# Kernel tuning notes

Measured on AMD Instinct MI355X. Metric: run time of the kernel, lower is better.

Reference implementation:

```python
import jax, jax.numpy as jnp
import numpy as np

N, E = 50000, 800000
F_IN, F_OUT, H, F_EDGE = 256, 32, 8, 5
LEAKY_SLOPE = 0.2


def setup_inputs() -> dict:
    key = jax.random.key(0)
    ks = jax.random.split(key, 6)
    x = jax.random.normal(ks[0], (N, F_IN), dtype=jnp.float32)
    edge_index = jax.random.randint(ks[1], (2, E), 0, N, dtype=jnp.int64)
    edge_attr = jax.random.normal(ks[2], (E, F_EDGE), dtype=jnp.float32)
    degree_src = jax.random.randint(ks[3], (E,), 0, 64, dtype=jnp.int64)
    # Xavier-uniform params
    lim_W = float(np.sqrt(6.0 / (F_IN + F_OUT)))
    W = jax.random.uniform(ks[4], (H, F_IN, F_OUT), minval=-lim_W, maxval=lim_W, dtype=jnp.float32)
    A = 2 * F_OUT + F_EDGE
    lim_a = float(np.sqrt(6.0 / (H + A)))
    a = jax.random.uniform(ks[5], (H, A), minval=-lim_a, maxval=lim_a, dtype=jnp.float32)
    lim_e = float(np.sqrt(1.0 / F_EDGE))
    W_edge_w = jax.random.uniform(jax.random.fold_in(key, 7), (F_EDGE, F_EDGE), minval=-lim_e, maxval=lim_e, dtype=jnp.float32)
    return {"x": x, "edge_index": edge_index, "edge_attr": edge_attr,
            "degree_src": degree_src, "W": W, "a": a, "W_edge_w": W_edge_w}


def reference(x, edge_index, edge_attr, degree_src, W, a, W_edge_w):
    n = x.shape[0]
    h, f_out = W.shape[0], W.shape[2]
    src, dst = edge_index[0], edge_index[1]
    # per-head projection: (N, H, F_out)
    Wh = jnp.einsum('nf,hfo->nho', x, W)
    # split attention vector instead of materializing the concat
    a_src, a_dst, a_e = a[:, :f_out], a[:, f_out:2 * f_out], a[:, 2 * f_out:]
    ef = edge_attr @ W_edge_w.T                      # (E, F_edge)
    e = (jnp.einsum('eho,ho->eh', Wh[src], a_src)
         + jnp.einsum('eho,ho->eh', Wh[dst], a_dst)
         + ef @ a_e.T)                                # (E, H)
    e = jax.nn.leaky_relu(e, LEAKY_SLOPE)
    scale = 1.0 / jnp.sqrt(jnp.clip(degree_src.astype(jnp.float32), 1.0, None))
    e = e * scale[:, None]
    # segment softmax over src; torch scatter_reduce amax include_self=True with zeros init -> max includes 0
    e_max = jnp.maximum(jax.ops.segment_max(e, src, num_segments=n), 0.0)
    e_exp = jnp.exp(e - e_max[src])
    e_sum = jax.ops.segment_sum(e_exp, src, num_segments=n)
    alpha = e_exp / (e_sum[src] + 1e-16)             # (E, H)
    msg = Wh[dst] * alpha[:, :, None]                # (E, H, F_out)
    out = jax.ops.segment_sum(msg, src, num_segments=n)
    out = jax.nn.elu(out.reshape(n, h * f_out))
    return out, alpha
```

## Files before the change

kernel.cpp:

```cpp
#include <hip/hip_runtime.h>
#include <hip/hip_bf16.h>
#include <math.h>

#define NN 50000
#define NE 800000
#define FIN 256
#define FOUT 32
#define NH 8
#define FE 5
#define AROW 69

typedef float f32x4 __attribute__((ext_vector_type(4)));
typedef short bf16x8 __attribute__((ext_vector_type(8)));

static __device__ __forceinline__ unsigned short f2bf(float f) {
    unsigned u = __float_as_uint(f);
    unsigned r = (u + 0x7FFFu + ((u >> 16) & 1u)) >> 16;
    return (unsigned short)r;
}
static __device__ __forceinline__ float bf2f(unsigned short b) {
    return __uint_as_float(((unsigned)b) << 16);
}

__global__ void k_cmat(const float* __restrict__ a, const float* __restrict__ Wew,
                       float* __restrict__ C) {
    int t = threadIdx.x;
    if (t < NH * FE) {
        int h = t / FE, k = t % FE;
        float s = 0.f;
        for (int j = 0; j < FE; ++j) s += a[h * AROW + 2 * FOUT + j] * Wew[j * FE + k];
        C[t] = s;
    }
}

__global__ __launch_bounds__(256) void k_prepB(const float* __restrict__ W,
                                               unsigned short* __restrict__ Bh,
                                               unsigned short* __restrict__ Bl) {
    int c = blockIdx.x;
    int k = threadIdx.x;
    int h = c >> 5, o = c & 31;
    float f = W[(size_t)h * (FIN * FOUT) + (size_t)k * FOUT + o];
    unsigned short hi = f2bf(f);
    unsigned short lo = f2bf(f - bf2f(hi));
    Bh[c * 256 + k] = hi;
    Bl[c * 256 + k] = lo;
}

__global__ __launch_bounds__(256) void k_gemm_mfma(const float* __restrict__ x,
                                                   const unsigned short* __restrict__ Bh,
                                                   const unsigned short* __restrict__ Bl,
                                                   const float* __restrict__ a,
                                                   unsigned short* __restrict__ Whb,
                                                   float* __restrict__ s1,
                                                   float* __restrict__ s2, int nrows) {
    __shared__ __align__(16) unsigned short Ah[64 * 56];
    int t = threadIdx.x;
    int w = t >> 6, l = t & 63;
    int r = l & 15, blk = l >> 4;
    int row0 = blockIdx.x * 64;
    int c0 = w * 64;

    f32x4 acc[4][4];
#pragma unroll
    for (int i = 0; i < 4; ++i)
#pragma unroll
        for (int j = 0; j < 4; ++j) acc[i][j] = (f32x4)(0.f);

    int srow = t >> 2, skq = (t & 3) * 8;
    const size_t xrow = (size_t)(row0 + srow) * FIN;

    for (int k0 = 0; k0 < FIN; k0 += 32) {
        {
            float v[8];
            if (row0 + srow < nrows) {
                f32x4 u0 = *(const f32x4*)&x[xrow + k0 + skq];
                f32x4 u1 = *(const f32x4*)&x[xrow + k0 + skq + 4];
                v[0] = u0.x; v[1] = u0.y; v[2] = u0.z; v[3] = u0.w;
                v[4] = u1.x; v[5] = u1.y; v[6] = u1.z; v[7] = u1.w;
            } else {
#pragma unroll
                for (int e = 0; e < 8; ++e) v[e] = 0.f;
            }
            bf16x8 hi;
#pragma unroll
            for (int e = 0; e < 8; ++e) hi[e] = (short)f2bf(v[e]);
            *(bf16x8*)&Ah[srow * 56 + skq] = hi;
        }
        __syncthreads();
        bf16x8 ah[4];
#pragma unroll
        for (int rt = 0; rt < 4; ++rt)
            ah[rt] = *(const bf16x8*)&Ah[(rt * 16 + r) * 56 + blk * 8];
#pragma unroll
        for (int ct = 0; ct < 4; ++ct) {
            int c = c0 + ct * 16 + r;
            bf16x8 bh = *(const bf16x8*)&Bh[c * 256 + k0 + blk * 8];
            bf16x8 bl = *(const bf16x8*)&Bl[c * 256 + k0 + blk * 8];
#pragma unroll
            for (int rt = 0; rt < 4; ++rt) {
                acc[rt][ct] = __builtin_amdgcn_mfma_f32_16x16x32_bf16(ah[rt], bh, acc[rt][ct], 0, 0, 0);
                acc[rt][ct] = __builtin_amdgcn_mfma_f32_16x16x32_bf16(ah[rt], bl, acc[rt][ct], 0, 0, 0);
            }
        }
        __syncthreads();
    }

#pragma unroll
    for (int rt = 0; rt < 4; ++rt) {
#pragma unroll
        for (int reg = 0; reg < 4; ++reg) {
            int row = row0 + rt * 16 + blk * 4 + reg;
            if (row < nrows) {
#pragma unroll
                for (int ct = 0; ct < 4; ++ct)
                    Whb[(size_t)row * 256 + c0 + ct * 16 + r] = f2bf(acc[rt][ct][reg]);
            }
        }
    }
    int h0 = 2 * w, h1 = 2 * w + 1;
    float as0 = a[h0 * AROW + r],       as0b = a[h0 * AROW + 16 + r];
    float ad0 = a[h0 * AROW + 32 + r],  ad0b = a[h0 * AROW + 48 + r];
    float as1 = a[h1 * AROW + r],       as1b = a[h1 * AROW + 16 + r];
    float ad1 = a[h1 * AROW + 32 + r],  ad1b = a[h1 * AROW + 48 + r];
#pragma unroll
    for (int rt = 0; rt < 4; ++rt) {
#pragma unroll
        for (int reg = 0; reg < 4; ++reg) {
            float p10 = acc[rt][0][reg] * as0 + acc[rt][1][reg] * as0b;
            float p20 = acc[rt][0][reg] * ad0 + acc[rt][1][reg] * ad0b;
            float p11 = acc[rt][2][reg] * as1 + acc[rt][3][reg] * as1b;
            float p21 = acc[rt][2][reg] * ad1 + acc[rt][3][reg] * ad1b;
#pragma unroll
            for (int d = 1; d < 16; d <<= 1) {
                p10 += __shfl_xor(p10, d);
                p20 += __shfl_xor(p20, d);
                p11 += __shfl_xor(p11, d);
                p21 += __shfl_xor(p21, d);
            }
            int row = row0 + rt * 16 + blk * 4 + reg;
            if (r == 0 && row < nrows) {
                s1[row * NH + h0] = p10;
                s2[row * NH + h0] = p20;
                s1[row * NH + h1] = p11;
                s2[row * NH + h1] = p21;
            }
        }
    }
}

__global__ __launch_bounds__(256) void k_count(const int* __restrict__ ei,
                                               int* __restrict__ counts) {
    int e = blockIdx.x * 256 + threadIdx.x;
    if (e < NE) atomicAdd(&counts[ei[e]], 1);
}

__global__ __launch_bounds__(256) void k_scanA(const int* __restrict__ counts,
                                               int* __restrict__ part,
                                               int* __restrict__ bsums, int n) {
    __shared__ int lds[256];
    int t = threadIdx.x;
    int base = blockIdx.x * 1024;
    int i0 = base + t * 4;
    int v0 = (i0 + 0 < n) ? counts[i0 + 0] : 0;
    int v1 = (i0 + 1 < n) ? counts[i0 + 1] : 0;
    int v2 = (i0 + 2 < n) ? counts[i0 + 2] : 0;
    int v3 = (i0 + 3 < n) ? counts[i0 + 3] : 0;
    int l0 = v0, l1 = l0 + v1, l2 = l1 + v2, l3 = l2 + v3;
    lds[t] = l3;
    __syncthreads();
    for (int off = 1; off < 256; off <<= 1) {
        int val = lds[t];
        if (t >= off) val += lds[t - off];
        __syncthreads();
        lds[t] = val;
        __syncthreads();
    }
    int excl = (t == 0) ? 0 : lds[t - 1];
    if (i0 + 0 < n) part[i0 + 0] = excl;
    if (i0 + 1 < n) part[i0 + 1] = excl + l0;
    if (i0 + 2 < n) part[i0 + 2] = excl + l1;
    if (i0 + 3 < n) part[i0 + 3] = excl + l2;
    if (t == 255) bsums[blockIdx.x] = lds[255];
}

__global__ void k_scanB(const int* __restrict__ bsums, int* __restrict__ boffs, int nb) {
    if (threadIdx.x == 0) {
        int run = 0;
        for (int b = 0; b < nb; ++b) { boffs[b] = run; run += bsums[b]; }
    }
}

__global__ __launch_bounds__(256) void k_scanC(int* __restrict__ row_ptr,
                                               const int* __restrict__ boffs, int n, int total) {
    int i = blockIdx.x * 256 + threadIdx.x;
    if (i < n) row_ptr[i] += boffs[i >> 10];
    else if (i == n) row_ptr[n] = total;
}

__global__ __launch_bounds__(256) void k_scatlog(const int* __restrict__ ei,
                                                 const float* __restrict__ eattr,
                                                 const int* __restrict__ degs,
                                                 const float* __restrict__ s1,
                                                 const float* __restrict__ s2,
                                                 const float* __restrict__ C,
                                                 const int* __restrict__ row_ptr,
                                                 int* __restrict__ fill,
                                                 float* __restrict__ e_perm,
                                                 int2* __restrict__ de_perm) {
    __shared__ float Cl[NH * FE];
    int t = threadIdx.x;
    if (t < NH * FE) Cl[t] = C[t];
    __syncthreads();
    int e = blockIdx.x * 256 + t;
    if (e >= NE) return;
    int src = ei[e], dst = ei[NE + e];
    int dg = degs[e];
    float scale = rsqrtf((float)(dg > 1 ? dg : 1));
    float ea0 = eattr[(size_t)e * FE + 0];
    float ea1 = eattr[(size_t)e * FE + 1];
    float ea2 = eattr[(size_t)e * FE + 2];
    float ea3 = eattr[(size_t)e * FE + 3];
    float ea4 = eattr[(size_t)e * FE + 4];
    float4 s1a = *(const float4*)&s1[src * NH];
    float4 s1b = *(const float4*)&s1[src * NH + 4];
    float4 s2a = *(const float4*)&s2[dst * NH];
    float4 s2b = *(const float4*)&s2[dst * NH + 4];
    float vs1[8] = {s1a.x, s1a.y, s1a.z, s1a.w, s1b.x, s1b.y, s1b.z, s1b.w};
    float vs2[8] = {s2a.x, s2a.y, s2a.z, s2a.w, s2b.x, s2b.y, s2b.z, s2b.w};
    float v[8];
#pragma unroll
    for (int h = 0; h < NH; ++h) {
        float q = vs1[h] + vs2[h] + ea0 * Cl[h * FE + 0] + ea1 * Cl[h * FE + 1] +
                  ea2 * Cl[h * FE + 2] + ea3 * Cl[h * FE + 3] + ea4 * Cl[h * FE + 4];
        q = q > 0.f ? q : 0.2f * q;
        v[h] = q * scale;
    }
    int p = row_ptr[src] + atomicAdd(&fill[src], 1);
    *(float4*)&e_perm[(size_t)p * 8]     = make_float4(v[0], v[1], v[2], v[3]);
    *(float4*)&e_perm[(size_t)p * 8 + 4] = make_float4(v[4], v[5], v[6], v[7]);
    de_perm[p] = make_int2(dst, e);
}

__global__ __launch_bounds__(256) void k_smmsg(const int* __restrict__ row_ptr,
                                               const float* __restrict__ e_perm,
                                               const int2* __restrict__ de_perm,
                                               const unsigned short* __restrict__ Whb,
                                               float* __restrict__ out_alpha,
                                               float* __restrict__ out) {
    __shared__ float m_s[NH], inv_s[NH];
    __shared__ float redv[4][NH];
    __shared__ int dl[32];
    __shared__ float al[256];
    int n = blockIdx.x;
    int t = threadIdx.x;
    int w = t >> 6;
    int start = row_ptr[n], deg = row_ptr[n + 1] - start;
    int j = t >> 3, h = t & 7;
    float v0 = (j < deg) ? e_perm[(size_t)(start + j) * 8 + h] : 0.f;
    float mx = fmaxf(v0, 0.f);
    for (int b = 32 + j; b < deg; b += 32)
        mx = fmaxf(mx, e_perm[(size_t)(start + b) * 8 + h]);
    mx = fmaxf(mx, __shfl_xor(mx, 8));
    mx = fmaxf(mx, __shfl_xor(mx, 16));
    mx = fmaxf(mx, __shfl_xor(mx, 32));
    if ((t & 63) < 8) redv[w][t & 63] = mx;
    __syncthreads();
    if (t < 8) m_s[t] = fmaxf(fmaxf(redv[0][t], redv[1][t]), fmaxf(redv[2][t], redv[3][t]));
    __syncthreads();
    float m = m_s[h];
    float ex0 = (j < deg) ? __expf(v0 - m) : 0.f;
    float sm = ex0;
    for (int b = 32 + j; b < deg; b += 32)
        sm += __expf(e_perm[(size_t)(start + b) * 8 + h] - m);
    sm += __shfl_xor(sm, 8);
    sm += __shfl_xor(sm, 16);
    sm += __shfl_xor(sm, 32);
    if ((t & 63) < 8) redv[w][t & 63] = sm;
    __syncthreads();
    if (t < 8) inv_s[t] = 1.f / (redv[0][t] + redv[1][t] + redv[2][t] + redv[3][t] + 1e-16f);
    __syncthreads();
    float accv = 0.f;
    int hh = t >> 5;
    for (int base = 0; base < deg; base += 32) {
        int cnt = deg - base;
        if (cnt > 32) cnt = 32;
        if (t < cnt) dl[t] = de_perm[start + base + t].x;
        if (t < cnt * 8) {
            size_t p = (size_t)(start + base + j);
            float av;
            if (base == 0) av = ex0 * inv_s[h];
            else           av = __expf(e_perm[p * 8 + h] - m_s[h]) * inv_s[h];
            al[t] = av;
            out_alpha[(size_t)de_perm[p].y * 8 + h] = av;
        }
        __syncthreads();
        for (int jj = 0; jj < cnt; ++jj)
            accv += al[jj * 8 + hh] * bf2f(Whb[(size_t)dl[jj] * 256 + t]);
        __syncthreads();
    }
    out[(size_t)n * 256 + t] = accv > 0.f ? accv : expm1f(accv);
}

extern "C" void kernel_launch(void* const* d_in, const int* in_sizes, int n_in,
                              void* d_out, int out_size, void* d_ws, size_t ws_size,
                              hipStream_t stream) {
    const float* x     = (const float*)d_in[0];
    const int*   ei    = (const int*)d_in[1];
    const float* eattr = (const float*)d_in[2];
    const int*   degs  = (const int*)d_in[3];
    const float* W     = (const float*)d_in[4];
    const float* a     = (const float*)d_in[5];
    const float* Wew   = (const float*)d_in[6];

    float* out       = (float*)d_out;
    float* out_alpha = out + (size_t)NN * 256;

    char* p = (char*)d_ws;
    auto alloc = [&](size_t bytes) -> char* {
        char* r = p;
        p += (bytes + 255) & ~(size_t)255;
        return r;
    };
    unsigned short* Whb     = (unsigned short*)alloc((size_t)NN * 256 * 2);
    float*          s1      = (float*)alloc((size_t)NN * NH * 4);
    float*          s2      = (float*)alloc((size_t)NN * NH * 4);
    float*          Cm      = (float*)alloc(NH * FE * 4);
    unsigned short* Bh      = (unsigned short*)alloc((size_t)256 * 256 * 2);
    unsigned short* Bl      = (unsigned short*)alloc((size_t)256 * 256 * 2);
    int*            counts  = (int*)alloc((size_t)NN * 4);
    int*            row_ptr = (int*)alloc((size_t)(NN + 1) * 4);
    int*            fill    = (int*)alloc((size_t)NN * 4);
    int*            bsums   = (int*)alloc(64 * 4);
    int*            boffs   = (int*)alloc(64 * 4);
    float*          e_perm  = (float*)alloc((size_t)NE * NH * 4);
    int2*           de_perm = (int2*)alloc((size_t)NE * 8);

    hipMemsetAsync(counts, 0, (size_t)NN * 4, stream);
    hipMemsetAsync(fill, 0, (size_t)NN * 4, stream);

    k_cmat<<<1, 64, 0, stream>>>(a, Wew, Cm);
    k_prepB<<<256, 256, 0, stream>>>(W, Bh, Bl);
    k_gemm_mfma<<<(NN + 63) / 64, 256, 0, stream>>>(x, Bh, Bl, a, Whb, s1, s2, NN);
    k_count<<<(NE + 255) / 256, 256, 0, stream>>>(ei, counts);
    k_scanA<<<(NN + 1023) / 1024, 256, 0, stream>>>(counts, row_ptr, bsums, NN);
    k_scanB<<<1, 64, 0, stream>>>(bsums, boffs, (NN + 1023) / 1024);
    k_scanC<<<(NN + 1 + 255) / 256, 256, 0, stream>>>(row_ptr, boffs, NN, NE);
    k_scatlog<<<(NE + 255) / 256, 256, 0, stream>>>(ei, eattr, degs, s1, s2, Cm,
                                                    row_ptr, fill, e_perm, de_perm);
    k_smmsg<<<NN, 256, 0, stream>>>(row_ptr, e_perm, de_perm, Whb, out_alpha, out);
}
```

Before: 274.2 us.

## Process one source node per wavefront in segment softmax-message kernel

Restructures the softmax/aggregation kernel so each 64-lane wavefront handles one source node instead of a 256-thread block per node. This removes block-wide __syncthreads and shared-memory reductions in favour of wave shuffles and per-wave LDS buffers with s_waitcnt fences. Each lane now accumulates 4 output features using vectorized ushort4 bf16 loads and a float4 store. The change cuts launched blocks by 4x and barrier overhead. In exchange, each lane does more serial work for high-degree nodes, and correctness relies on intra-wave LDS ordering without a barrier.

```diff
diff --git a/kernel.cpp b/kernel.cpp
--- a/kernel.cpp
+++ b/kernel.cpp
@@ -247,58 +247,80 @@
                                                const unsigned short* __restrict__ Whb,
                                                float* __restrict__ out_alpha,
                                                float* __restrict__ out) {
-    __shared__ float m_s[NH], inv_s[NH];
-    __shared__ float redv[4][NH];
-    __shared__ int dl[32];
-    __shared__ float al[256];
-    int n = blockIdx.x;
-    int t = threadIdx.x;
-    int w = t >> 6;
+    __shared__ float al[4][256];
+    __shared__ int dl[4][32];
+    __shared__ int el[4][32];
+    int t = threadIdx.x;
+    int w = t >> 6, l = t & 63;
+    int n = blockIdx.x * 4 + w;
+    if (n >= NN) return;
     int start = row_ptr[n], deg = row_ptr[n + 1] - start;
-    int j = t >> 3, h = t & 7;
-    float v0 = (j < deg) ? e_perm[(size_t)(start + j) * 8 + h] : 0.f;
-    float mx = fmaxf(v0, 0.f);
-    for (int b = 32 + j; b < deg; b += 32)
+    int j = l >> 3, h = l & 7;
+
+    float vc[4];
+#pragma unroll
+    for (int q = 0; q < 4; ++q) {
+        int b = j + 8 * q;
+        vc[q] = (b < deg) ? e_perm[(size_t)(start + b) * 8 + h] : -1e30f;
+    }
+    float mx = 0.f;
+#pragma unroll
+    for (int q = 0; q < 4; ++q) mx = fmaxf(mx, vc[q]);
+    for (int b = 32 + j; b < deg; b += 8)
         mx = fmaxf(mx, e_perm[(size_t)(start + b) * 8 + h]);
     mx = fmaxf(mx, __shfl_xor(mx, 8));
     mx = fmaxf(mx, __shfl_xor(mx, 16));
     mx = fmaxf(mx, __shfl_xor(mx, 32));
-    if ((t & 63) < 8) redv[w][t & 63] = mx;
-    __syncthreads();
-    if (t < 8) m_s[t] = fmaxf(fmaxf(redv[0][t], redv[1][t]), fmaxf(redv[2][t], redv[3][t]));
-    __syncthreads();
-    float m = m_s[h];
-    float ex0 = (j < deg) ? __expf(v0 - m) : 0.f;
-    float sm = ex0;
-    for (int b = 32 + j; b < deg; b += 32)
+    float m = mx;
+    float ex[4];
+    float sm = 0.f;
+#pragma unroll
+    for (int q = 0; q < 4; ++q) { ex[q] = __expf(vc[q] - m); sm += ex[q]; }
+    for (int b = 32 + j; b < deg; b += 8)
         sm += __expf(e_perm[(size_t)(start + b) * 8 + h] - m);
     sm += __shfl_xor(sm, 8);
     sm += __shfl_xor(sm, 16);
     sm += __shfl_xor(sm, 32);
-    if ((t & 63) < 8) redv[w][t & 63] = sm;
-    __syncthreads();
-    if (t < 8) inv_s[t] = 1.f / (redv[0][t] + redv[1][t] + redv[2][t] + redv[3][t] + 1e-16f);
-    __syncthreads();
-    float accv = 0.f;
-    int hh = t >> 5;
+    float inv = 1.f / (sm + 1e-16f);
+    f32x4 acc = (f32x4)(0.f);
+    int hh = l >> 3;
     for (int base = 0; base < deg; base += 32) {
         int cnt = deg - base;
         if (cnt > 32) cnt = 32;
-        if (t < cnt) dl[t] = de_perm[start + base + t].x;
-        if (t < cnt * 8) {
-            size_t p = (size_t)(start + base + j);
-            float av;
-            if (base == 0) av = ex0 * inv_s[h];
-            else           av = __expf(e_perm[p * 8 + h] - m_s[h]) * inv_s[h];
-            al[t] = av;
-            out_alpha[(size_t)de_perm[p].y * 8 + h] = av;
-        }
-        __syncthreads();
-        for (int jj = 0; jj < cnt; ++jj)
-            accv += al[jj * 8 + hh] * bf2f(Whb[(size_t)dl[jj] * 256 + t]);
-        __syncthreads();
-    }
-    out[(size_t)n * 256 + t] = accv > 0.f ? accv : expm1f(accv);
+        if (l < cnt) {
+            int2 de = de_perm[start + base + l];
+            dl[w][l] = de.x;
+            el[w][l] = de.y;
+        }
+        asm volatile("s_waitcnt lgkmcnt(0)" ::: "memory");
+#pragma unroll
+        for (int q = 0; q < 4; ++q) {
+            int b = base + j + 8 * q;
+            if (b < deg) {
+                float av = (base == 0 ? ex[q]
+                                      : __expf(e_perm[(size_t)(start + b) * 8 + h] - m)) * inv;
+                al[w][(j + 8 * q) * 8 + h] = av;
+                out_alpha[(size_t)el[w][j + 8 * q] * 8 + h] = av;
+            }
+        }
+        asm volatile("s_waitcnt lgkmcnt(0)" ::: "memory");
+        for (int jj = 0; jj < cnt; ++jj) {
+            int d = dl[w][jj];
+            float av = al[w][jj * 8 + hh];
+            ushort4 u = *(const ushort4*)&Whb[(size_t)d * 256 + l * 4];
+            acc.x += av * bf2f(u.x);
+            acc.y += av * bf2f(u.y);
+            acc.z += av * bf2f(u.z);
+            acc.w += av * bf2f(u.w);
+        }
+        asm volatile("s_waitcnt lgkmcnt(0)" ::: "memory");
+    }
+    f32x4 o;
+    o.x = acc.x > 0.f ? acc.x : expm1f(acc.x);
+    o.y = acc.y > 0.f ? acc.y : expm1f(acc.y);
+    o.z = acc.z > 0.f ? acc.z : expm1f(acc.z);
+    o.w = acc.w > 0.f ? acc.w : expm1f(acc.w);
+    *(f32x4*)&out[(size_t)n * 256 + l * 4] = o;
 }
 
 extern "C" void kernel_launch(void* const* d_in, const int* in_sizes, int n_in,
@@ -347,5 +369,6 @@
     k_scanC<<<(NN + 1 + 255) / 256, 256, 0, stream>>>(row_ptr, boffs, NN, NE);
     k_scatlog<<<(NE + 255) / 256, 256, 0, stream>>>(ei, eattr, degs, s1, s2, Cm,
                                                     row_ptr, fill, e_perm, de_perm);
-    k_smmsg<<<NN, 256, 0, stream>>>(row_ptr, e_perm, de_perm, Whb, out_alpha, out);
-}
+    k_smmsg<<<(NN + 3) / 4, 256, 0, stream>>>(row_ptr, e_perm, de_perm, Whb,
+                                              out_alpha, out);
+}
```

Measured after the change: 235.4 us. 1.16x faster.
